# Kernel tuning notes

Hardware: AMD Instinct MI355X
Metric: run time of the kernel (lower is better)

Reference implementation:

```python
import jax, jax.numpy as jnp
import numpy as np

EMB = 256
D_INNER = 512                         # expand=2 * d_model
HEADDIM = 64
NHEADS = D_INNER // HEADDIM           # 8
DSTATE = 128
DCONV = 4
CONV_DIM = D_INNER + 2 * DSTATE       # 768 (ngroups=1)
D_IN_PROJ = 2 * D_INNER + 2 * DSTATE + NHEADS  # 1288
LN_EPS = 1e-5


def _layernorm(x, w, b):
    m = jnp.mean(x, axis=-1, keepdims=True)
    v = jnp.mean((x - m) ** 2, axis=-1, keepdims=True)
    return (x - m) * jax.lax.rsqrt(v + LN_EPS) * w + b


def _wn_linear(x, g, v, b):
    # torch weight_norm(dim=0): w = g * v / ||v|| per output row
    w = g[:, None] * v / jnp.linalg.norm(v, axis=1, keepdims=True)
    return x @ w.T + b


def _ssm_scan(x, dt, A, Bm, Cm):
    # x: (b,l,h,p)  dt: (b,l,h)  A: (h,)  Bm/Cm: (b,l,n)
    dA = jnp.exp(dt * A)           # (b,l,h), A<0 so dA in (0,1)
    dtx = dt[..., None] * x        # (b,l,h,p)
    bsz = x.shape[0]

    def step(h, inp):
        dA_t, dtx_t, B_t, C_t = inp
        h = h * dA_t[:, :, None, None] + dtx_t[..., None] * B_t[:, None, None, :]
        y = jnp.einsum('bhpn,bn->bhp', h, C_t)
        return h, y

    h0 = jnp.zeros((bsz, NHEADS, HEADDIM, DSTATE), x.dtype)
    xs = (jnp.swapaxes(dA, 0, 1), jnp.swapaxes(dtx, 0, 1),
          jnp.swapaxes(Bm, 0, 1), jnp.swapaxes(Cm, 0, 1))
    _, ys = jax.lax.scan(step, h0, xs)
    return jnp.swapaxes(ys, 0, 1)  # (b,l,h,p)


def _mamba2(u, in_proj_w, conv_w, conv_b, dt_bias, A_log, D_param, ssm_norm_w, out_proj_w):
    B, L, _ = u.shape
    zxbcdt = u @ in_proj_w.T                       # (B,L,1288)
    z_gate = zxbcdt[..., :D_INNER]
    xBC = zxbcdt[..., D_INNER:D_INNER + CONV_DIM]
    dt = zxbcdt[..., D_INNER + CONV_DIM:]
    # causal depthwise conv1d
    xp = jnp.pad(xBC, ((0, 0), (DCONV - 1, 0), (0, 0)))
    xc = jax.lax.conv_general_dilated(
        jnp.swapaxes(xp, 1, 2), conv_w[:, None, :], (1,), 'VALID',
        feature_group_count=CONV_DIM, dimension_numbers=('NCH', 'OIH', 'NCH'))
    xc = jax.nn.silu(jnp.swapaxes(xc, 1, 2) + conv_b)
    x = xc[..., :D_INNER].reshape(B, L, NHEADS, HEADDIM)
    Bm = xc[..., D_INNER:D_INNER + DSTATE]
    Cm = xc[..., D_INNER + DSTATE:]
    dt = jax.nn.softplus(dt + dt_bias)             # (B,L,H)
    A = -jnp.exp(A_log)                            # (H,)
    y = _ssm_scan(x, dt, A, Bm, Cm) + D_param[None, None, :, None] * x
    y = y.reshape(B, L, D_INNER)
    # gated RMSNorm (norm_before_gate=False): rmsnorm(y * silu(z)) * w
    yg = y * jax.nn.silu(z_gate)
    yn = yg * jax.lax.rsqrt(jnp.mean(yg ** 2, axis=-1, keepdims=True) + LN_EPS) * ssm_norm_w
    return yn @ out_proj_w.T


def setup_inputs() -> dict:
    key = jax.random.key(0)
    ks = jax.random.split(key, 12)
    B, NU, NA = 1, 64, 512

    def rn(k, shape, scale):
        return jax.random.normal(k, shape, dtype=jnp.float32) * scale

    z = rn(ks[0], (B, NU, NA, EMB), 1.0)
    in_proj_w = rn(ks[1], (D_IN_PROJ, EMB), EMB ** -0.5)
    conv_w = rn(ks[2], (CONV_DIM, DCONV), DCONV ** -0.5)
    conv_b = rn(ks[3], (CONV_DIM,), 0.02)
    dt_bias = jnp.log(jnp.expm1(jax.random.uniform(ks[4], (NHEADS,), minval=0.001, maxval=0.1)))
    A_log = jnp.log(jax.random.uniform(ks[5], (NHEADS,), minval=1.0, maxval=16.0))
    D_param = jnp.ones((NHEADS,), dtype=jnp.float32)
    ssm_norm_w = jnp.ones((D_INNER,), dtype=jnp.float32)
    out_proj_w = rn(ks[6], (EMB, D_INNER), D_INNER ** -0.5)
    ff_v = rn(ks[7], (EMB, EMB), EMB ** -0.5)
    ff_g = jnp.linalg.norm(ff_v, axis=1)
    ff_b = jnp.zeros((EMB,), dtype=jnp.float32)
    fc1_v = rn(ks[8], (EMB, EMB), EMB ** -0.5)
    fc1_g = jnp.linalg.norm(fc1_v, axis=1)
    fc1_b = jnp.zeros((EMB,), dtype=jnp.float32)
    fc2_v = rn(ks[9], (EMB, EMB), EMB ** -0.5)
    fc2_g = jnp.linalg.norm(fc2_v, axis=1)
    fc2_b = jnp.zeros((EMB,), dtype=jnp.float32)
    return {
        'z': z,
        'ln1_w': jnp.ones((EMB,), dtype=jnp.float32), 'ln1_b': jnp.zeros((EMB,), dtype=jnp.float32),
        'in_proj_w': in_proj_w, 'conv_w': conv_w, 'conv_b': conv_b,
        'dt_bias': dt_bias, 'A_log': A_log, 'D_param': D_param,
        'ssm_norm_w': ssm_norm_w, 'out_proj_w': out_proj_w,
        'ff_g': ff_g, 'ff_v': ff_v, 'ff_b': ff_b,
        'ln2_w': jnp.ones((EMB,), dtype=jnp.float32), 'ln2_b': jnp.zeros((EMB,), dtype=jnp.float32),
        'fc1_g': fc1_g, 'fc1_v': fc1_v, 'fc1_b': fc1_b,
        'fc2_g': fc2_g, 'fc2_v': fc2_v, 'fc2_b': fc2_b,
    }


def reference(z, ln1_w, ln1_b, in_proj_w, conv_w, conv_b, dt_bias, A_log, D_param,
              ssm_norm_w, out_proj_w, ff_g, ff_v, ff_b, ln2_w, ln2_b,
              fc1_g, fc1_v, fc1_b, fc2_g, fc2_v, fc2_b):
    b, nu, na, e = z.shape
    # MambaBlock: z + ff(mamba(norm(z)))
    u = _layernorm(z, ln1_w, ln1_b).reshape(-1, na, e)
    y = _mamba2(u, in_proj_w, conv_w, conv_b, dt_bias, A_log, D_param, ssm_norm_w, out_proj_w)
    y = _wn_linear(y, ff_g, ff_v, ff_b).reshape(b, nu, na, e)
    z = z + y
    # NormFF: z + Lin2(GELU(Lin1(LN(z))))  (dropout inactive in eval)
    h = _layernorm(z, ln2_w, ln2_b)
    h = jax.nn.gelu(_wn_linear(h, fc1_g, fc1_v, fc1_b), approximate=False)
    h = _wn_linear(h, fc2_g, fc2_v, fc2_b)
    return z + h
```

## Files before the change

### kernel.cpp

```cpp
#include <hip/hip_runtime.h>
#include <stdint.h>
#include <math.h>

#define EMB       256
#define D_INNER   512
#define HEADDIM   64
#define NHEADS    8
#define DSTATE    128
#define DCONV     4
#define CONV_DIM  768
#define LN_EPS    1e-5f
#define NBATCH    64
#define SEQLEN    512
#define NTOK      (NBATCH*SEQLEN)

typedef __attribute__((ext_vector_type(8))) short          short8;
typedef __attribute__((ext_vector_type(8))) unsigned short u16x8;
typedef __attribute__((ext_vector_type(4))) unsigned short u16x4;
typedef __attribute__((ext_vector_type(4))) float          f32x4;

__device__ __forceinline__ float bfb(unsigned short u) {
    union { unsigned int i; float f; } x; x.i = ((unsigned int)u) << 16; return x.f;
}
__device__ __forceinline__ unsigned short fbf(float f) {
    union { float f; unsigned int i; } x; x.f = f;
    unsigned int i = x.i;
    unsigned int lsb = (i >> 16) & 1u;
    i += 0x7fffu + lsb;
    return (unsigned short)(i >> 16);
}

__device__ __forceinline__ void gld16(const unsigned short* g, unsigned short* l) {
    __builtin_amdgcn_global_load_lds((const __attribute__((address_space(1))) void*)g,
                                     (__attribute__((address_space(3))) void*)l, 16, 0, 0);
}

__global__ __launch_bounds__(256) void cvt_k(const float* __restrict__ in,
                                             unsigned short* __restrict__ out, int n) {
    int i = blockIdx.x * 256 + threadIdx.x;
    if (i < n) out[i] = fbf(in[i]);
}

__global__ __launch_bounds__(256) void ln_k(const float* __restrict__ in,
                                            const float* __restrict__ w,
                                            const float* __restrict__ b,
                                            unsigned short* __restrict__ out) {
    int tok = blockIdx.x, tid = threadIdx.x;
    size_t idx = (size_t)tok * 256 + tid;
    float x = in[idx];
    __shared__ float sm[8];
    float s = x;
    #pragma unroll
    for (int o = 32; o; o >>= 1) s += __shfl_down(s, o);
    if ((tid & 63) == 0) sm[tid >> 6] = s;
    __syncthreads();
    float mean = (sm[0] + sm[1] + sm[2] + sm[3]) * (1.f / 256.f);
    float d = x - mean;
    float q = d * d;
    #pragma unroll
    for (int o = 32; o; o >>= 1) q += __shfl_down(q, o);
    if ((tid & 63) == 0) sm[4 + (tid >> 6)] = q;
    __syncthreads();
    float var = (sm[4] + sm[5] + sm[6] + sm[7]) * (1.f / 256.f);
    out[idx] = fbf(d * rsqrtf(var + LN_EPS) * w[tid] + b[tid]);
}

__global__ __launch_bounds__(256) void wnorm_k(const float* __restrict__ g,
                                               const float* __restrict__ v,
                                               unsigned short* __restrict__ wout) {
    int o = blockIdx.x, tid = threadIdx.x;
    float x = v[(size_t)o * 256 + tid];
    float q = x * x;
    __shared__ float sm[4];
    #pragma unroll
    for (int d = 32; d; d >>= 1) q += __shfl_down(q, d);
    if ((tid & 63) == 0) sm[tid >> 6] = q;
    __syncthreads();
    float tot = sm[0] + sm[1] + sm[2] + sm[3];
    float scale = g[o] * rsqrtf(tot);
    wout[(size_t)o * 256 + tid] = fbf(x * scale);
}

#define BMT 128
#define BNT 128
#define BKT 32
template<int EPI, int NBN>
__global__ __launch_bounds__(256) void gemm_k(const unsigned short* __restrict__ A,
                                              const unsigned short* __restrict__ Bw,
                                              int K, int N,
                                              unsigned short* __restrict__ out_b,
                                              float* __restrict__ out_f,
                                              const float* __restrict__ bias,
                                              const float* __restrict__ res_f,
                                              unsigned short* __restrict__ out2_b) {
    __shared__ __align__(16) unsigned short smem[16384];
    int tid = threadIdx.x;
    int d = blockIdx.x;
    const int cpx = (256 * NBN) >> 3;
    int logical = (d & 7) * cpx + (d >> 3);
    int bm = logical / NBN;
    int bn = logical % NBN;
    int lane = tid & 63, w = tid >> 6;
    int wr = w >> 1, wc = w & 1;
    int fr = lane & 15, fq = lane >> 4;

    int rsub = w * 16 + (lane >> 2);
    int cl   = ((lane & 3) ^ ((rsub >> 1) & 3)) << 3;
    const unsigned short* gA0 = A  + (size_t)(bm * BMT + rsub)      * K + cl;
    const unsigned short* gA1 = A  + (size_t)(bm * BMT + rsub + 64) * K + cl;
    const unsigned short* gB0 = Bw + (size_t)(bn * BNT + rsub)      * K + cl;
    const unsigned short* gB1 = Bw + (size_t)(bn * BNT + rsub + 64) * K + cl;

    f32x4 acc[4][4];
    #pragma unroll
    for (int m = 0; m < 4; m++)
        #pragma unroll
        for (int n = 0; n < 4; n++)
            #pragma unroll
            for (int r = 0; r < 4; r++) acc[m][n][r] = 0.f;

    auto AS = [&](int buf) { return &smem[buf * 4096]; };
    auto BS = [&](int buf) { return &smem[8192 + buf * 4096]; };
    auto STAGE = [&](int buf, int k0) {
        gld16(gA0 + k0, AS(buf) + w * 512);
        gld16(gA1 + k0, AS(buf) + 2048 + w * 512);
        gld16(gB0 + k0, BS(buf) + w * 512);
        gld16(gB1 + k0, BS(buf) + 2048 + w * 512);
    };

    int nt = K / BKT;
    STAGE(0, 0);
    asm volatile("s_waitcnt vmcnt(0)" ::: "memory");
    __builtin_amdgcn_s_barrier();
    for (int t = 0; t < nt; ++t) {
        int buf = t & 1;
        if (t + 1 < nt) STAGE(buf ^ 1, (t + 1) * BKT);
        short8 af[4], bf_[4];
        #pragma unroll
        for (int m = 0; m < 4; m++) {
            int ra = wr * 64 + m * 16 + fr;
            af[m] = *(const short8*)&AS(buf)[ra * 32 + ((fq ^ ((ra >> 1) & 3)) << 3)];
        }
        #pragma unroll
        for (int n = 0; n < 4; n++) {
            int rb = wc * 64 + n * 16 + fr;
            bf_[n] = *(const short8*)&BS(buf)[rb * 32 + ((fq ^ ((rb >> 1) & 3)) << 3)];
        }
        #pragma unroll
        for (int m = 0; m < 4; m++)
            #pragma unroll
            for (int n = 0; n < 4; n++)
                acc[m][n] = __builtin_amdgcn_mfma_f32_16x16x32_bf16(af[m], bf_[n], acc[m][n], 0, 0, 0);
        asm volatile("s_waitcnt vmcnt(0)" ::: "memory");
        __builtin_amdgcn_s_barrier();
    }

    if (EPI == 1 && bn == 10) {
        #pragma unroll
        for (int m = 0; m < 4; m++)
            #pragma unroll
            for (int n = 0; n < 4; n++)
                #pragma unroll
                for (int r = 0; r < 4; r++) {
                    int grow = bm * BMT + wr * 64 + m * 16 + fq * 4 + r;
                    int gcol = 1280 + wc * 64 + n * 16 + fr;
                    if (gcol < 1288) {
                        float a2 = acc[m][n][r] + bias[gcol - 1280];
                        out_f[(size_t)grow * 8 + (gcol - 1280)] =
                            a2 > 20.f ? a2 : log1pf(expf(a2));
                    }
                }
    } else if (EPI == 0 || EPI == 1) {
        unsigned short* cb = smem;
        #pragma unroll
        for (int s = 0; s < 2; s++) {
            if (wr == s) {
                #pragma unroll
                for (int m = 0; m < 4; m++)
                    #pragma unroll
                    for (int n = 0; n < 4; n++)
                        #pragma unroll
                        for (int r = 0; r < 4; r++)
                            cb[(m * 16 + fq * 4 + r) * 136 + wc * 64 + n * 16 + fr] =
                                fbf(acc[m][n][r]);
            }
            __syncthreads();
            #pragma unroll
            for (int k = 0; k < 4; k++) {
                int g = k * 256 + tid;
                int row = g >> 4, col = (g & 15) << 3;
                u16x8 v = *(const u16x8*)&cb[row * 136 + col];
                int grow = bm * BMT + s * 64 + row;
                int gc = bn * BNT + col;
                if (EPI == 0) {
                    *(u16x8*)&out_b[(size_t)grow * N + gc] = v;
                } else {
                    if (gc < 512) *(u16x8*)&out_b[(size_t)grow * 512 + gc] = v;
                    else          *(u16x8*)&out2_b[(size_t)grow * 768 + (gc - 512)] = v;
                }
            }
            __syncthreads();
        }
    } else {
        float* fb = (float*)smem;
        #pragma unroll
        for (int s = 0; s < 4; s++) {
            if (wr == (s >> 1)) {
                int mp = s & 1;
                #pragma unroll
                for (int mm = 0; mm < 2; mm++)
                    #pragma unroll
                    for (int n = 0; n < 4; n++)
                        #pragma unroll
                        for (int r = 0; r < 4; r++)
                            fb[(mm * 16 + fq * 4 + r) * 132 + wc * 64 + n * 16 + fr] =
                                acc[mp * 2 + mm][n][r];
            }
            __syncthreads();
            #pragma unroll
            for (int k = 0; k < 4; k++) {
                int g = k * 256 + tid;
                int row = g >> 5, col = (g & 31) << 2;
                f32x4 v = *(const f32x4*)&fb[row * 132 + col];
                int grow = bm * BMT + (s >> 1) * 64 + (s & 1) * 32 + row;
                int gc = bn * BNT + col;
                size_t idx = (size_t)grow * 256 + gc;
                if (EPI == 2) {
                    f32x4 rr = *(const f32x4*)&res_f[idx];
                    f32x4 o;
                    #pragma unroll
                    for (int j = 0; j < 4; j++) o[j] = rr[j] + v[j] + bias[gc + j];
                    *(f32x4*)&out_f[idx] = o;
                } else {
                    u16x4 o;
                    #pragma unroll
                    for (int j = 0; j < 4; j++) {
                        float x = v[j] + bias[gc + j];
                        o[j] = fbf(0.5f * x * (1.f + erff(x * 0.70710678118654752f)));
                    }
                    *(u16x4*)&out_b[idx] = o;
                }
            }
            __syncthreads();
        }
    }
}

__global__ __launch_bounds__(256) void conv_k(unsigned short* xbc,
                                              const float* __restrict__ cw,
                                              const float* __restrict__ cb) {
    int b = blockIdx.y;
    int c0 = blockIdx.x * 64;
    int tid = threadIdx.x;
    int c = tid & 63;
    int rq = tid >> 6;
    __shared__ unsigned short sraw[131][72];
    int ca = c0 + c;
    float w0 = cw[ca * 4 + 0], w1 = cw[ca * 4 + 1];
    float w2 = cw[ca * 4 + 2], w3 = cw[ca * 4 + 3];
    float bias = cb[ca];
    unsigned short carry_u = 0;

    for (int t0 = 0; t0 < 512; t0 += 128) {
        __syncthreads();
        if (tid < 192) sraw[rq][c] = carry_u;
        for (int idx = tid; idx < 1024; idx += 256) {
            int lt = idx >> 3, cg = idx & 7;
            *(u16x8*)&sraw[3 + lt][cg * 8] =
                *(const u16x8*)&xbc[((size_t)(b * 512 + t0 + lt)) * 768 + c0 + cg * 8];
        }
        __syncthreads();
        if (tid < 192) carry_u = sraw[128 + rq][c];
        #pragma unroll 4
        for (int i = 0; i < 32; i++) {
            int lt = rq + 4 * i;
            float acc = bias
                + bfb(sraw[lt + 0][c]) * w0
                + bfb(sraw[lt + 1][c]) * w1
                + bfb(sraw[lt + 2][c]) * w2
                + bfb(sraw[lt + 3][c]) * w3;
            acc = acc / (1.f + expf(-acc));
            xbc[((size_t)(b * 512 + t0 + lt)) * 768 + c0 + c] = fbf(acc);
        }
    }
}

#define CPAD 136
#define TPAD 48
#define TOFF(r) ((((r) >> 4) & 1) << 3)
__global__ __launch_bounds__(256) void ssd_k(const unsigned short* __restrict__ xc,
                                             const float* __restrict__ dts,
                                             const float* __restrict__ A_log,
                                             const float* __restrict__ D_param,
                                             unsigned short* __restrict__ y) {
    __shared__ unsigned short Ct[32][CPAD];
    __shared__ unsigned short Bt[32][CPAD];
    __shared__ unsigned short BtT[128][TPAD];
    __shared__ unsigned short XT[64][TPAD];
    __shared__ unsigned short DXT[64][TPAD];
    __shared__ unsigned short DXWT[64][TPAD];
    __shared__ unsigned short LG[32][40];
    __shared__ unsigned short hB[64][CPAD];
    __shared__ unsigned short Yb[32][72];
    __shared__ float scum[32], sdt2[32], sEC[32];
    __shared__ float sET[32][36];

    int bh = blockIdx.x;
    int b = bh >> 3, h = bh & 7;
    int tid = threadIdx.x;
    int w = tid >> 6;
    int lane = tid & 63;
    int fr = lane & 15, fq = lane >> 4;

    float A_h = -expf(A_log[h]);
    float D_h = D_param[h];

    f32x4 hacc[8];
    #pragma unroll
    for (int nf = 0; nf < 8; nf++)
        #pragma unroll
        for (int r = 0; r < 4; r++) hacc[nf][r] = 0.f;

    int t  = tid >> 3;
    int e8 = tid & 7;

    for (int c = 0; c < 16; ++c) {
        size_t tok0 = (size_t)b * 512 + c * 32;
        u16x8 bv0, bv1, cv0, cv1, xv;
        {
            const unsigned short* row = &xc[(tok0 + t) * 768];
            bv0 = *(const u16x8*)&row[512 + e8 * 16];
            bv1 = *(const u16x8*)&row[512 + e8 * 16 + 8];
            cv0 = *(const u16x8*)&row[640 + e8 * 16];
            cv1 = *(const u16x8*)&row[640 + e8 * 16 + 8];
            xv  = *(const u16x8*)&row[h * 64 + e8 * 8];
        }
        *(u16x8*)&Ct[t][e8 * 16]     = cv0;
        *(u16x8*)&Ct[t][e8 * 16 + 8] = cv1;
        *(u16x8*)&Bt[t][e8 * 16]     = bv0;
        *(u16x8*)&Bt[t][e8 * 16 + 8] = bv1;
        {
            int tof = TOFF(e8 * 16);
            #pragma unroll
            for (int j = 0; j < 8; j++) {
                BtT[e8 * 16 + j][t + tof]     = bv0[j];
                BtT[e8 * 16 + 8 + j][t + tof] = bv1[j];
            }
            #pragma unroll
            for (int j = 0; j < 8; j++)
                XT[e8 * 8 + j][t + TOFF(e8 * 8 + j)] = xv[j];
        }
        if (tid < 32) {
            float dtv = dts[(tok0 + tid) * 8 + h];
            sdt2[tid] = dtv;
            float la = dtv * A_h;
            #pragma unroll
            for (int dd = 1; dd < 32; dd <<= 1) {
                float up = __shfl_up(la, dd);
                if (lane >= dd) la += up;
            }
            scum[tid] = la;
        }
        __syncthreads();
        float cumQ = scum[31];
        if (tid < 32) sEC[tid] = expf(scum[tid]);
        {
            float dtv = sdt2[t];
            float wgt = expf(cumQ - scum[t]);
            #pragma unroll
            for (int j = 0; j < 8; j++) {
                float dtx = dtv * bfb(xv[j]);
                int rr = e8 * 8 + j;
                DXT[rr][t + TOFF(rr)]  = fbf(dtx);
                DXWT[rr][t + TOFF(rr)] = fbf(wgt * dtx);
            }
        }
        #pragma unroll
        for (int k = 0; k < 4; k++) {
            int idx = tid * 4 + k;
            int tt = idx >> 5, tq = idx & 31;
            sET[tt][tq] = (tq <= tt) ? expf(scum[tt] - scum[tq]) : 0.f;
        }
        #pragma unroll
        for (int nf = 0; nf < 8; nf++)
            #pragma unroll
            for (int r = 0; r < 4; r++)
                hB[w * 16 + fq * 4 + r][nf * 16 + fr] = fbf(hacc[nf][r]);
        __syncthreads();
        {
            int m = w >> 1, nf = w & 1;
            f32x4 g;
            #pragma unroll
            for (int r = 0; r < 4; r++) g[r] = 0.f;
            #pragma unroll
            for (int ks = 0; ks < 4; ks++) {
                short8 ca = *(const short8*)&Ct[m * 16 + fr][ks * 32 + fq * 8];
                short8 bb = *(const short8*)&Bt[nf * 16 + fr][ks * 32 + fq * 8];
                g = __builtin_amdgcn_mfma_f32_16x16x32_bf16(ca, bb, g, 0, 0, 0);
            }
            #pragma unroll
            for (int r = 0; r < 4; r++) {
                int tt = m * 16 + fq * 4 + r;
                int tq = nf * 16 + fr;
                LG[tt][tq] = fbf(g[r] * sET[tt][tq]);
            }
        }
        __syncthreads();
        f32x4 Yi[2];
        #pragma unroll
        for (int m = 0; m < 2; m++)
            #pragma unroll
            for (int r = 0; r < 4; r++) Yi[m][r] = 0.f;
        #pragma unroll
        for (int ks = 0; ks < 4; ks++) {
            short8 a0 = *(const short8*)&Ct[fr][ks * 32 + fq * 8];
            short8 a1 = *(const short8*)&Ct[16 + fr][ks * 32 + fq * 8];
            short8 hb = *(const short8*)&hB[w * 16 + fr][ks * 32 + fq * 8];
            Yi[0] = __builtin_amdgcn_mfma_f32_16x16x32_bf16(a0, hb, Yi[0], 0, 0, 0);
            Yi[1] = __builtin_amdgcn_mfma_f32_16x16x32_bf16(a1, hb, Yi[1], 0, 0, 0);
        }
        #pragma unroll
        for (int m = 0; m < 2; m++)
            #pragma unroll
            for (int r = 0; r < 4; r++) Yi[m][r] *= sEC[m * 16 + fq * 4 + r];
        {
            int wof = (w & 1) << 3;
            short8 a0 = *(const short8*)&LG[fr][fq * 8];
            short8 a1 = *(const short8*)&LG[16 + fr][fq * 8];
            short8 dx = *(const short8*)&DXT[w * 16 + fr][fq * 8 + wof];
            Yi[0] = __builtin_amdgcn_mfma_f32_16x16x32_bf16(a0, dx, Yi[0], 0, 0, 0);
            Yi[1] = __builtin_amdgcn_mfma_f32_16x16x32_bf16(a1, dx, Yi[1], 0, 0, 0);
        }
        {
            float ecq = sEC[31];
            #pragma unroll
            for (int nf = 0; nf < 8; nf++)
                #pragma unroll
                for (int r = 0; r < 4; r++) hacc[nf][r] *= ecq;
            int wof = (w & 1) << 3;
            short8 ax = *(const short8*)&DXWT[w * 16 + fr][fq * 8 + wof];
            #pragma unroll
            for (int nf = 0; nf < 8; nf++) {
                short8 bb = *(const short8*)&BtT[nf * 16 + fr][fq * 8 + ((nf & 1) << 3)];
                hacc[nf] = __builtin_amdgcn_mfma_f32_16x16x32_bf16(ax, bb, hacc[nf], 0, 0, 0);
            }
        }
        {
            int wof = (w & 1) << 3;
            #pragma unroll
            for (int m = 0; m < 2; m++)
                #pragma unroll
                for (int r = 0; r < 4; r++) {
                    int tt = m * 16 + fq * 4 + r;
                    float xf = bfb(XT[w * 16 + fr][tt + wof]);
                    Yb[tt][w * 16 + fr] = fbf(Yi[m][r] + D_h * xf);
                }
        }
        __syncthreads();
        {
            u16x8 yv = *(const u16x8*)&Yb[t][e8 * 8];
            *(u16x8*)&y[(tok0 + t) * 512 + h * 64 + e8 * 8] = yv;
        }
    }
}

__global__ __launch_bounds__(256) void gate_k(const unsigned short* __restrict__ y,
                                              const unsigned short* __restrict__ zg,
                                              const float* __restrict__ nw,
                                              unsigned short* __restrict__ yn) {
    int tok = blockIdx.x, tid = threadIdx.x;
    size_t base = (size_t)tok * 512;
    float gv[2];
    float q = 0.f;
    #pragma unroll
    for (int j = 0; j < 2; j++) {
        int c = tid + j * 256;
        float yy = bfb(y[base + c]);
        float zz = bfb(zg[base + c]);
        float s = zz / (1.f + expf(-zz));
        float t = yy * s;
        gv[j] = t;
        q += t * t;
    }
    __shared__ float sm[4];
    #pragma unroll
    for (int o = 32; o; o >>= 1) q += __shfl_down(q, o);
    if ((tid & 63) == 0) sm[tid >> 6] = q;
    __syncthreads();
    float ms = (sm[0] + sm[1] + sm[2] + sm[3]) * (1.f / 512.f);
    float r = rsqrtf(ms + LN_EPS);
    #pragma unroll
    for (int j = 0; j < 2; j++) {
        int c = tid + j * 256;
        yn[base + c] = fbf(gv[j] * r * nw[c]);
    }
}

extern "C" void kernel_launch(void* const* d_in, const int* in_sizes, int n_in,
                              void* d_out, int out_size, void* d_ws, size_t ws_size,
                              hipStream_t stream) {
    if (n_in < 22) return;
    static const int setup_sizes[22] = {8388608,256,256,329728,3072,768,8,8,8,512,
                                        131072,256,65536,256,256,256,256,65536,256,256,65536,256};
    for (int i = 0; i < 22; i++) if (in_sizes[i] != setup_sizes[i]) return;

    const float* z      = (const float*)d_in[0];
    const float* ln1w   = (const float*)d_in[1];
    const float* ln1b   = (const float*)d_in[2];
    const float* inW    = (const float*)d_in[3];
    const float* convw  = (const float*)d_in[4];
    const float* convb  = (const float*)d_in[5];
    const float* dtb    = (const float*)d_in[6];
    const float* Alog   = (const float*)d_in[7];
    const float* Dp     = (const float*)d_in[8];
    const float* normw  = (const float*)d_in[9];
    const float* outW   = (const float*)d_in[10];
    const float* ffg    = (const float*)d_in[11];
    const float* ffv    = (const float*)d_in[12];
    const float* ffb    = (const float*)d_in[13];
    const float* ln2w   = (const float*)d_in[14];
    const float* ln2b   = (const float*)d_in[15];
    const float* fc1g   = (const float*)d_in[16];
    const float* fc1v   = (const float*)d_in[17];
    const float* fc1b   = (const float*)d_in[18];
    const float* fc2g   = (const float*)d_in[19];
    const float* fc2v   = (const float*)d_in[20];
    const float* fc2b   = (const float*)d_in[21];
    float* out = (float*)d_out;
    (void)out_size;

    char* ws = (char*)d_ws;
    const size_t SLOT_A = (size_t)NTOK * 768 * 2;
    const size_t SLOT_B = (size_t)NTOK * 512 * 2;
    const size_t SLOT_C = (size_t)NTOK * 512 * 2;
    const size_t SLOT_D = (size_t)NTOK * 256 * 2;
    const size_t SLOT_E = (size_t)NTOK * 8 * 4;
    const size_t SLOT_W = (size_t)256 * 256 * 2;
    const size_t SLOT_WI = (size_t)1288 * 256 * 2;
    const size_t SLOT_WO = (size_t)256 * 512 * 2;
    char* pA = ws;
    char* pB = pA + SLOT_A;
    char* pC = pB + SLOT_B;
    char* pD = pC + SLOT_C;
    char* pE = pD + SLOT_D;
    char* pW = pE + SLOT_E;
    char* pWI = pW + 3 * SLOT_W;
    char* pWO = pWI + SLOT_WI;
    size_t need = SLOT_A + SLOT_B + SLOT_C + SLOT_D + SLOT_E + 3 * SLOT_W + SLOT_WI + SLOT_WO;
    if (ws_size < need) return;

    unsigned short* xbc = (unsigned short*)pA;
    unsigned short* yn  = (unsigned short*)pA;
    unsigned short* t2  = (unsigned short*)(pA + (size_t)NTOK * 512 * 2);
    unsigned short* y   = (unsigned short*)pB;
    float*          z2  = (float*)pB;
    unsigned short* zgb = (unsigned short*)pC;
    unsigned short* u   = (unsigned short*)pD;
    unsigned short* m1  = (unsigned short*)pD;
    unsigned short* h1  = (unsigned short*)pD;
    float*          dts = (float*)pE;
    unsigned short* wff  = (unsigned short*)pW;
    unsigned short* wfc1 = (unsigned short*)(pW + SLOT_W);
    unsigned short* wfc2 = (unsigned short*)(pW + 2 * SLOT_W);
    unsigned short* inWb = (unsigned short*)pWI;
    unsigned short* outWb = (unsigned short*)pWO;

    cvt_k<<<(1288 * 256 + 255) / 256, 256, 0, stream>>>(inW, inWb, 1288 * 256);
    cvt_k<<<(256 * 512 + 255) / 256, 256, 0, stream>>>(outW, outWb, 256 * 512);
    wnorm_k<<<256, 256, 0, stream>>>(ffg,  ffv,  wff);
    wnorm_k<<<256, 256, 0, stream>>>(fc1g, fc1v, wfc1);
    wnorm_k<<<256, 256, 0, stream>>>(fc2g, fc2v, wfc2);
    ln_k<<<NTOK, 256, 0, stream>>>(z, ln1w, ln1b, u);
    gemm_k<1, 11><<<256 * 11, 256, 0, stream>>>(u, inWb, 256, 1288,
                                                zgb, dts, dtb, nullptr, xbc);
    conv_k<<<dim3(12, 64), 256, 0, stream>>>(xbc, convw, convb);
    ssd_k<<<NBATCH * NHEADS, 256, 0, stream>>>(xbc, dts, Alog, Dp, y);
    gate_k<<<NTOK, 256, 0, stream>>>(y, zgb, normw, yn);
    gemm_k<0, 2><<<256 * 2, 256, 0, stream>>>(yn, outWb, 512, 256,
                                              m1, nullptr, nullptr, nullptr, nullptr);
    gemm_k<2, 2><<<256 * 2, 256, 0, stream>>>(m1, wff, 256, 256,
                                              nullptr, z2, ffb, z, nullptr);
    ln_k<<<NTOK, 256, 0, stream>>>(z2, ln2w, ln2b, t2);
    gemm_k<3, 2><<<256 * 2, 256, 0, stream>>>(t2, wfc1, 256, 256,
                                              h1, nullptr, fc1b, nullptr, nullptr);
    gemm_k<2, 2><<<256 * 2, 256, 0, stream>>>(h1, wfc2, 256, 256,
                                              nullptr, out, fc2b, z2, nullptr);
}
```

Before: 342.6 us.

## Fold out_proj into ff weight, fuse weight prep kernels, trim SSD shared buffers

Precomputes the product of the ff weight and the out_proj weight so the two consecutive token-wide GEMMs collapse into one GEMM with K=512, removing an intermediate write and read plus a kernel launch. The small weight conversion and weight-norm launches are merged into single kernels. In the SSD kernel the decay weighting is moved from a separate DXWT buffer onto the transposed B tile, which drops one shared buffer, and the transpose padding is widened to cut bank conflicts. Folding the two weights rounds their product to bf16 once, which changes the numerics slightly, and the new folding kernel is a naive per-call matmul.

```diff
diff --git a/kernel.cpp b/kernel.cpp
--- a/kernel.cpp
+++ b/kernel.cpp
@@ -35,10 +35,47 @@
                                      (__attribute__((address_space(3))) void*)l, 16, 0, 0);
 }
 
-__global__ __launch_bounds__(256) void cvt_k(const float* __restrict__ in,
-                                             unsigned short* __restrict__ out, int n) {
+__global__ __launch_bounds__(256) void cvt2_k(const float* __restrict__ a, unsigned short* __restrict__ oa, int na,
+                                              const float* __restrict__ b, unsigned short* __restrict__ ob, int nb) {
     int i = blockIdx.x * 256 + threadIdx.x;
-    if (i < n) out[i] = fbf(in[i]);
+    if (i < na) oa[i] = fbf(a[i]);
+    else { i -= na; if (i < nb) ob[i] = fbf(b[i]); }
+}
+
+__global__ __launch_bounds__(256) void wnorm3_k(const float* __restrict__ g0, const float* __restrict__ v0, unsigned short* __restrict__ o0,
+                                                const float* __restrict__ g1, const float* __restrict__ v1, unsigned short* __restrict__ o1,
+                                                const float* __restrict__ g2, const float* __restrict__ v2, unsigned short* __restrict__ o2) {
+    int o = blockIdx.x & 255, s = blockIdx.x >> 8, tid = threadIdx.x;
+    const float* g = s == 0 ? g0 : (s == 1 ? g1 : g2);
+    const float* v = s == 0 ? v0 : (s == 1 ? v1 : v2);
+    unsigned short* wout = s == 0 ? o0 : (s == 1 ? o1 : o2);
+    float x = v[(size_t)o * 256 + tid];
+    float q = x * x;
+    __shared__ float sm[4];
+    #pragma unroll
+    for (int d = 32; d; d >>= 1) q += __shfl_down(q, d);
+    if ((tid & 63) == 0) sm[tid >> 6] = q;
+    __syncthreads();
+    float tot = sm[0] + sm[1] + sm[2] + sm[3];
+    float scale = g[o] * rsqrtf(tot);
+    wout[(size_t)o * 256 + tid] = fbf(x * scale);
+}
+
+__global__ __launch_bounds__(256) void wco_k(const unsigned short* __restrict__ wff,
+                                             const unsigned short* __restrict__ outWb,
+                                             unsigned short* __restrict__ wco) {
+    int i = blockIdx.x, tid = threadIdx.x;
+    __shared__ float row[256];
+    row[tid] = bfb(wff[(size_t)i * 256 + tid]);
+    __syncthreads();
+    #pragma unroll
+    for (int half = 0; half < 2; half++) {
+        int k = tid + half * 256;
+        float acc = 0.f;
+        for (int j = 0; j < 256; j++)
+            acc += row[j] * bfb(outWb[(size_t)j * 512 + k]);
+        wco[(size_t)i * 512 + k] = fbf(acc);
+    }
 }
 
 __global__ __launch_bounds__(256) void ln_k(const float* __restrict__ in,
@@ -63,22 +100,6 @@
     __syncthreads();
     float var = (sm[4] + sm[5] + sm[6] + sm[7]) * (1.f / 256.f);
     out[idx] = fbf(d * rsqrtf(var + LN_EPS) * w[tid] + b[tid]);
-}
-
-__global__ __launch_bounds__(256) void wnorm_k(const float* __restrict__ g,
-                                               const float* __restrict__ v,
-                                               unsigned short* __restrict__ wout) {
-    int o = blockIdx.x, tid = threadIdx.x;
-    float x = v[(size_t)o * 256 + tid];
-    float q = x * x;
-    __shared__ float sm[4];
-    #pragma unroll
-    for (int d = 32; d; d >>= 1) q += __shfl_down(q, d);
-    if ((tid & 63) == 0) sm[tid >> 6] = q;
-    __syncthreads();
-    float tot = sm[0] + sm[1] + sm[2] + sm[3];
-    float scale = g[o] * rsqrtf(tot);
-    wout[(size_t)o * 256 + tid] = fbf(x * scale);
 }
 
 #define BMT 128
@@ -286,8 +307,8 @@
 }
 
 #define CPAD 136
-#define TPAD 48
-#define TOFF(r) ((((r) >> 4) & 1) << 3)
+#define TPAD 56
+#define TOFF(r) ((((r) >> 4) & 3) << 3)
 __global__ __launch_bounds__(256) void ssd_k(const unsigned short* __restrict__ xc,
                                              const float* __restrict__ dts,
                                              const float* __restrict__ A_log,
@@ -298,7 +319,6 @@
     __shared__ unsigned short BtT[128][TPAD];
     __shared__ unsigned short XT[64][TPAD];
     __shared__ unsigned short DXT[64][TPAD];
-    __shared__ unsigned short DXWT[64][TPAD];
     __shared__ unsigned short LG[32][40];
     __shared__ unsigned short hB[64][CPAD];
     __shared__ unsigned short Yb[32][72];
@@ -339,17 +359,9 @@
         *(u16x8*)&Ct[t][e8 * 16 + 8] = cv1;
         *(u16x8*)&Bt[t][e8 * 16]     = bv0;
         *(u16x8*)&Bt[t][e8 * 16 + 8] = bv1;
-        {
-            int tof = TOFF(e8 * 16);
-            #pragma unroll
-            for (int j = 0; j < 8; j++) {
-                BtT[e8 * 16 + j][t + tof]     = bv0[j];
-                BtT[e8 * 16 + 8 + j][t + tof] = bv1[j];
-            }
-            #pragma unroll
-            for (int j = 0; j < 8; j++)
-                XT[e8 * 8 + j][t + TOFF(e8 * 8 + j)] = xv[j];
-        }
+        #pragma unroll
+        for (int j = 0; j < 8; j++)
+            XT[e8 * 8 + j][t + TOFF(e8 * 8 + j)] = xv[j];
         if (tid < 32) {
             float dtv = dts[(tok0 + tid) * 8 + h];
             sdt2[tid] = dtv;
@@ -367,12 +379,14 @@
         {
             float dtv = sdt2[t];
             float wgt = expf(cumQ - scum[t]);
+            int tof = TOFF(e8 * 16);
             #pragma unroll
             for (int j = 0; j < 8; j++) {
                 float dtx = dtv * bfb(xv[j]);
                 int rr = e8 * 8 + j;
-                DXT[rr][t + TOFF(rr)]  = fbf(dtx);
-                DXWT[rr][t + TOFF(rr)] = fbf(wgt * dtx);
+                DXT[rr][t + TOFF(rr)] = fbf(dtx);
+                BtT[e8 * 16 + j][t + tof]     = fbf(wgt * bfb(bv0[j]));
+                BtT[e8 * 16 + 8 + j][t + tof] = fbf(wgt * bfb(bv1[j]));
             }
         }
         #pragma unroll
@@ -424,7 +438,7 @@
             #pragma unroll
             for (int r = 0; r < 4; r++) Yi[m][r] *= sEC[m * 16 + fq * 4 + r];
         {
-            int wof = (w & 1) << 3;
+            int wof = TOFF(w * 16);
             short8 a0 = *(const short8*)&LG[fr][fq * 8];
             short8 a1 = *(const short8*)&LG[16 + fr][fq * 8];
             short8 dx = *(const short8*)&DXT[w * 16 + fr][fq * 8 + wof];
@@ -437,16 +451,16 @@
             for (int nf = 0; nf < 8; nf++)
                 #pragma unroll
                 for (int r = 0; r < 4; r++) hacc[nf][r] *= ecq;
-            int wof = (w & 1) << 3;
-            short8 ax = *(const short8*)&DXWT[w * 16 + fr][fq * 8 + wof];
+            int wof = TOFF(w * 16);
+            short8 ax = *(const short8*)&DXT[w * 16 + fr][fq * 8 + wof];
             #pragma unroll
             for (int nf = 0; nf < 8; nf++) {
-                short8 bb = *(const short8*)&BtT[nf * 16 + fr][fq * 8 + ((nf & 1) << 3)];
+                short8 bb = *(const short8*)&BtT[nf * 16 + fr][fq * 8 + TOFF(nf * 16)];
                 hacc[nf] = __builtin_amdgcn_mfma_f32_16x16x32_bf16(ax, bb, hacc[nf], 0, 0, 0);
             }
         }
         {
-            int wof = (w & 1) << 3;
+            int wof = TOFF(w * 16);
             #pragma unroll
             for (int m = 0; m < 2; m++)
                 #pragma unroll
@@ -538,6 +552,7 @@
     const size_t SLOT_W = (size_t)256 * 256 * 2;
     const size_t SLOT_WI = (size_t)1288 * 256 * 2;
     const size_t SLOT_WO = (size_t)256 * 512 * 2;
+    const size_t SLOT_WC = (size_t)256 * 512 * 2;
     char* pA = ws;
     char* pB = pA + SLOT_A;
     char* pC = pB + SLOT_B;
@@ -546,7 +561,8 @@
     char* pW = pE + SLOT_E;
     char* pWI = pW + 3 * SLOT_W;
     char* pWO = pWI + SLOT_WI;
-    size_t need = SLOT_A + SLOT_B + SLOT_C + SLOT_D + SLOT_E + 3 * SLOT_W + SLOT_WI + SLOT_WO;
+    char* pWC = pWO + SLOT_WO;
+    size_t need = SLOT_A + SLOT_B + SLOT_C + SLOT_D + SLOT_E + 3 * SLOT_W + SLOT_WI + SLOT_WO + SLOT_WC;
     if (ws_size < need) return;
 
     unsigned short* xbc = (unsigned short*)pA;
@@ -556,7 +572,6 @@
     float*          z2  = (float*)pB;
     unsigned short* zgb = (unsigned short*)pC;
     unsigned short* u   = (unsigned short*)pD;
-    unsigned short* m1  = (unsigned short*)pD;
     unsigned short* h1  = (unsigned short*)pD;
     float*          dts = (float*)pE;
     unsigned short* wff  = (unsigned short*)pW;
@@ -564,21 +579,19 @@
     unsigned short* wfc2 = (unsigned short*)(pW + 2 * SLOT_W);
     unsigned short* inWb = (unsigned short*)pWI;
     unsigned short* outWb = (unsigned short*)pWO;
-
-    cvt_k<<<(1288 * 256 + 255) / 256, 256, 0, stream>>>(inW, inWb, 1288 * 256);
-    cvt_k<<<(256 * 512 + 255) / 256, 256, 0, stream>>>(outW, outWb, 256 * 512);
-    wnorm_k<<<256, 256, 0, stream>>>(ffg,  ffv,  wff);
-    wnorm_k<<<256, 256, 0, stream>>>(fc1g, fc1v, wfc1);
-    wnorm_k<<<256, 256, 0, stream>>>(fc2g, fc2v, wfc2);
+    unsigned short* wco  = (unsigned short*)pWC;
+
+    cvt2_k<<<(1288 * 256 + 131072 + 255) / 256, 256, 0, stream>>>(inW, inWb, 1288 * 256,
+                                                                  outW, outWb, 131072);
+    wnorm3_k<<<768, 256, 0, stream>>>(ffg, ffv, wff, fc1g, fc1v, wfc1, fc2g, fc2v, wfc2);
+    wco_k<<<256, 256, 0, stream>>>(wff, outWb, wco);
     ln_k<<<NTOK, 256, 0, stream>>>(z, ln1w, ln1b, u);
     gemm_k<1, 11><<<256 * 11, 256, 0, stream>>>(u, inWb, 256, 1288,
                                                 zgb, dts, dtb, nullptr, xbc);
     conv_k<<<dim3(12, 64), 256, 0, stream>>>(xbc, convw, convb);
     ssd_k<<<NBATCH * NHEADS, 256, 0, stream>>>(xbc, dts, Alog, Dp, y);
     gate_k<<<NTOK, 256, 0, stream>>>(y, zgb, normw, yn);
-    gemm_k<0, 2><<<256 * 2, 256, 0, stream>>>(yn, outWb, 512, 256,
-                                              m1, nullptr, nullptr, nullptr, nullptr);
-    gemm_k<2, 2><<<256 * 2, 256, 0, stream>>>(m1, wff, 256, 256,
+    gemm_k<2, 2><<<256 * 2, 256, 0, stream>>>(yn, wco, 512, 256,
                                               nullptr, z2, ffb, z, nullptr);
     ln_k<<<NTOK, 256, 0, stream>>>(z2, ln2w, ln2b, t2);
     gemm_k<3, 2><<<256 * 2, 256, 0, stream>>>(t2, wfc1, 256, 256,
```

Result: faster. 320.1 us (-6.6%).
